# Kernel tuning notes

Measured on AMD Instinct MI355X. Metric: run time of the kernel, lower is better.

## Reference

```python
import jax, jax.numpy as jnp
import numpy as np

N = 4096
E_EDGES = 262144
F_IN = 128      # num_features
H = 4           # nhead (GAT heads and MHA heads)
C = 64          # d_model (per-head GAT out dim)
EMB = H * C     # 256, MHA embed_dim
DFF = 128       # dim_feedforward
HD = EMB // H   # MHA head dim = 64


def setup_inputs() -> dict:
    key = jax.random.key(0)
    ks = jax.random.split(key, 16)
    inp = {}
    inp["tgt"] = jax.random.normal(ks[0], (N, F_IN), jnp.float32)
    inp["memory"] = jax.random.normal(ks[1], (N, EMB), jnp.float32)
    inp["original_signal"] = jax.random.normal(ks[2], (N, EMB), jnp.float32)
    inp["edge_index"] = jax.random.randint(ks[3], (2, E_EDGES), 0, N, jnp.int32)
    # GATConv params (PyG: lin has no bias; separate bias of size H*C; att vectors [1,H,C])
    s = 1.0 / np.sqrt(F_IN)
    inp["W_gat"] = jax.random.normal(ks[4], (F_IN, H * C), jnp.float32) * s
    inp["att_src"] = jax.random.normal(ks[5], (H, C), jnp.float32) * (1.0 / np.sqrt(C))
    inp["att_dst"] = jax.random.normal(ks[6], (H, C), jnp.float32) * (1.0 / np.sqrt(C))
    inp["b_gat"] = jnp.zeros((H * C,), jnp.float32)
    # nn.MultiheadAttention params
    se = 1.0 / np.sqrt(EMB)
    inp["in_proj_w"] = jax.random.normal(ks[7], (3 * EMB, EMB), jnp.float32) * se
    inp["in_proj_b"] = jnp.zeros((3 * EMB,), jnp.float32)
    inp["out_proj_w"] = jax.random.normal(ks[8], (EMB, EMB), jnp.float32) * se
    inp["out_proj_b"] = jnp.zeros((EMB,), jnp.float32)
    # linear1
    inp["lin1_w"] = jax.random.normal(ks[9], (DFF, EMB), jnp.float32) * se
    inp["lin1_b"] = jnp.zeros((DFF,), jnp.float32)
    return inp


def _gat_conv(x, edge_index, W, att_src, att_dst, bias):
    n = x.shape[0]
    xh = (x @ W).reshape(n, H, C)                       # [N,H,C]
    a_s = jnp.sum(xh * att_src, axis=-1)                # [N,H]
    a_d = jnp.sum(xh * att_dst, axis=-1)                # [N,H]
    # add self loops (PyG default add_self_loops=True)
    loop = jnp.arange(n, dtype=edge_index.dtype)
    src = jnp.concatenate([edge_index[0], loop])
    dst = jnp.concatenate([edge_index[1], loop])
    alpha = jax.nn.leaky_relu(a_s[src] + a_d[dst], negative_slope=0.2)  # [E+N,H]
    # edge softmax grouped by destination node
    m = jax.ops.segment_max(alpha, dst, num_segments=n)
    alpha = jnp.exp(alpha - m[dst])
    denom = jax.ops.segment_sum(alpha, dst, num_segments=n)
    alpha = alpha / (denom[dst] + 1e-16)
    # message passing: weighted scatter-add of source features
    out = jax.ops.segment_sum(xh[src] * alpha[:, :, None], dst, num_segments=n)  # [N,H,C]
    return out.reshape(n, H * C) + bias


def _mha(q_in, k_in, v_in, in_proj_w, in_proj_b, out_proj_w, out_proj_b):
    # batch=1, seq=N; dropout inactive (eval)
    q = q_in @ in_proj_w[:EMB].T + in_proj_b[:EMB]
    k = k_in @ in_proj_w[EMB:2 * EMB].T + in_proj_b[EMB:2 * EMB]
    v = v_in @ in_proj_w[2 * EMB:].T + in_proj_b[2 * EMB:]
    q = q.reshape(-1, H, HD)
    k = k.reshape(-1, H, HD)
    v = v.reshape(-1, H, HD)
    scale = 1.0 / np.sqrt(HD)
    scores = jnp.einsum('nhd,mhd->hnm', q * scale, k)   # [H,N,N]
    attn = jax.nn.softmax(scores, axis=-1)
    o = jnp.einsum('hnm,mhd->nhd', attn, v).reshape(-1, EMB)
    return o @ out_proj_w.T + out_proj_b


def reference(tgt, memory, original_signal, edge_index,
              W_gat, att_src, att_dst, b_gat,
              in_proj_w, in_proj_b, out_proj_w, out_proj_b,
              lin1_w, lin1_b):
    t = _gat_conv(tgt, edge_index, W_gat, att_src, att_dst, b_gat)
    t = jax.nn.leaky_relu(t, negative_slope=0.01)       # F.leaky_relu default slope
    fused = _mha(t, memory, original_signal, in_proj_w, in_proj_b, out_proj_w, out_proj_b)
    return jax.nn.relu(fused @ lin1_w.T + lin1_b)       # [N, DFF]
```

## Files before the change

kernel.cpp:

```cpp
#include <hip/hip_runtime.h>

#define NN   4096
#define EE   262144
#define ET   (EE + NN)
#define HH   4
#define EMB  256
#define DFF  128
#define FIN  128
#define KSPLIT 8
#define KCHUNK (NN / KSPLIT)

typedef float  f32x16  __attribute__((ext_vector_type(16)));
typedef __bf16 bf16x8  __attribute__((ext_vector_type(8)));
typedef unsigned short u16;
typedef unsigned short u16x4 __attribute__((ext_vector_type(4)));

__device__ __forceinline__ u16 f2bf(float f) {
  unsigned u = __float_as_uint(f);
  u += 0x7fffu + ((u >> 16) & 1u);
  return (u16)(u >> 16);
}

__global__ __launch_bounds__(256) void gemm_f32(
    const float* __restrict__ A, const float* __restrict__ B,
    float* __restrict__ Cf, int M, int Nn, int K)
{
  __shared__ float As[64][17];
  __shared__ float Bs[16][65];
  const int tid = threadIdx.x;
  const int tr = tid >> 4, tc = tid & 15;
  const int m0 = blockIdx.y * 64, n0 = blockIdx.x * 64;
  float acc[4][4] = {};
  for (int k0 = 0; k0 < K; k0 += 16) {
    {
      const int r = tid >> 2, kq = (tid & 3) << 2;
      const float4 av = *(const float4*)(A + (size_t)(m0 + r) * K + k0 + kq);
      As[r][kq] = av.x; As[r][kq + 1] = av.y; As[r][kq + 2] = av.z; As[r][kq + 3] = av.w;
    }
    {
      const int kk = tid >> 4, jq = (tid & 15) << 2;
      const float4 bv = *(const float4*)(B + (size_t)(k0 + kk) * Nn + n0 + jq);
      Bs[kk][jq] = bv.x; Bs[kk][jq + 1] = bv.y; Bs[kk][jq + 2] = bv.z; Bs[kk][jq + 3] = bv.w;
    }
    __syncthreads();
#pragma unroll
    for (int kk = 0; kk < 16; ++kk) {
      float a[4], b[4];
#pragma unroll
      for (int i = 0; i < 4; ++i) a[i] = As[tr * 4 + i][kk];
#pragma unroll
      for (int j = 0; j < 4; ++j) b[j] = Bs[kk][tc * 4 + j];
#pragma unroll
      for (int i = 0; i < 4; ++i)
#pragma unroll
        for (int j = 0; j < 4; ++j) acc[i][j] += a[i] * b[j];
    }
    __syncthreads();
  }
#pragma unroll
  for (int i = 0; i < 4; ++i)
#pragma unroll
    for (int j = 0; j < 4; ++j)
      Cf[(size_t)(m0 + tr * 4 + i) * Nn + n0 + tc * 4 + j] = acc[i][j];
}

__global__ __launch_bounds__(256) void bgemm(
    const float* __restrict__ A, const float* __restrict__ B, const float* __restrict__ bias,
    float* __restrict__ Cf, int M, int Nn, int K, int act)
{
  __shared__ u16 As[64][40], Bs[64][40];
  const int tid = threadIdx.x;
  const int m0 = blockIdx.y * 64, n0 = blockIdx.x * 64;
  const int w = tid >> 6, l = tid & 63, lq = l & 31, hi = l >> 5;
  const int wm = w >> 1, wn = w & 1;
  f32x16 acc = {0};
  for (int k0 = 0; k0 < K; k0 += 32) {
    __syncthreads();
#pragma unroll
    for (int it = 0; it < 2; ++it) {
      const int idx = tid + it * 256;
      const int row = idx >> 3, slot = idx & 7;
      const float4 av = *(const float4*)(A + (size_t)(m0 + row) * K + k0 + slot * 4);
      u16x4 ap = {f2bf(av.x), f2bf(av.y), f2bf(av.z), f2bf(av.w)};
      *(u16x4*)(&As[row][slot * 4]) = ap;
      const float4 bv = *(const float4*)(B + (size_t)(n0 + row) * K + k0 + slot * 4);
      u16x4 bp = {f2bf(bv.x), f2bf(bv.y), f2bf(bv.z), f2bf(bv.w)};
      *(u16x4*)(&Bs[row][slot * 4]) = bp;
    }
    __syncthreads();
#pragma unroll
    for (int c = 0; c < 2; ++c) {
      const bf16x8 af = *(const bf16x8*)(&As[wm * 32 + lq][c * 16 + hi * 8]);
      const bf16x8 bf = *(const bf16x8*)(&Bs[wn * 32 + lq][c * 16 + hi * 8]);
      acc = __builtin_amdgcn_mfma_f32_32x32x16_bf16(af, bf, acc, 0, 0, 0);
    }
  }
  const int col = n0 + wn * 32 + lq;
  const float bcol = bias ? bias[col] : 0.f;
#pragma unroll
  for (int r = 0; r < 16; ++r) {
    const int row = m0 + wm * 32 + (r & 3) + 8 * (r >> 2) + 4 * hi;
    float v = acc[r] + bcol;
    if (act == 2) v = fmaxf(v, 0.f);
    Cf[(size_t)row * Nn + col] = v;
  }
}

__global__ __launch_bounds__(256) void qkv_mfma(
    const float* __restrict__ tbuf, const float* __restrict__ mem, const float* __restrict__ orig,
    const float* __restrict__ ipw, const float* __restrict__ ipb,
    u16* __restrict__ qb, u16* __restrict__ kbuf, u16* __restrict__ vT)
{
  __shared__ u16 As[64][40], Bs[64][40];
  const int z = blockIdx.z;
  const float* A = (z == 0) ? tbuf : (z == 1 ? mem : orig);
  const float* B = ipw + (size_t)z * EMB * EMB;
  const float* bias = ipb + z * EMB;
  const float oscale = (z == 0) ? 0.125f : 1.f;
  const int tid = threadIdx.x;
  const int m0 = blockIdx.y * 64, n0 = blockIdx.x * 64;
  const int w = tid >> 6, l = tid & 63, lq = l & 31, hi = l >> 5;
  const int wm = w >> 1, wn = w & 1;
  f32x16 acc = {0};
  for (int k0 = 0; k0 < EMB; k0 += 32) {
    __syncthreads();
#pragma unroll
    for (int it = 0; it < 2; ++it) {
      const int idx = tid + it * 256;
      const int row = idx >> 3, slot = idx & 7;
      const float4 av = *(const float4*)(A + (size_t)(m0 + row) * EMB + k0 + slot * 4);
      u16x4 ap = {f2bf(av.x), f2bf(av.y), f2bf(av.z), f2bf(av.w)};
      *(u16x4*)(&As[row][slot * 4]) = ap;
      const float4 bv = *(const float4*)(B + (size_t)(n0 + row) * EMB + k0 + slot * 4);
      u16x4 bp = {f2bf(bv.x), f2bf(bv.y), f2bf(bv.z), f2bf(bv.w)};
      *(u16x4*)(&Bs[row][slot * 4]) = bp;
    }
    __syncthreads();
#pragma unroll
    for (int c = 0; c < 2; ++c) {
      const bf16x8 af = *(const bf16x8*)(&As[wm * 32 + lq][c * 16 + hi * 8]);
      const bf16x8 bf = *(const bf16x8*)(&Bs[wn * 32 + lq][c * 16 + hi * 8]);
      acc = __builtin_amdgcn_mfma_f32_32x32x16_bf16(af, bf, acc, 0, 0, 0);
    }
  }
  const int col = n0 + wn * 32 + lq;
  const float bcol = bias[col];
  const int hh = col >> 6, dd = col & 63;
#pragma unroll
  for (int r = 0; r < 16; ++r) {
    const int row = m0 + wm * 32 + (r & 3) + 8 * (r >> 2) + 4 * hi;
    const u16 bw = f2bf((acc[r] + bcol) * oscale);
    if (z == 2) vT[((size_t)hh * 64 + dd) * NN + row] = bw;
    else if (z == 1) kbuf[((size_t)hh * NN + row) * 64 + dd] = bw;
    else qb[((size_t)hh * NN + row) * 64 + dd] = bw;
  }
}

__global__ __launch_bounds__(256) void att_sums(const float* __restrict__ xh,
                                                const float* __restrict__ att_src,
                                                const float* __restrict__ att_dst,
                                                float* __restrict__ a_s, float* __restrict__ a_d)
{
  const int n = blockIdx.x, t = threadIdx.x;
  const int h = t >> 6, c = t & 63;
  const float v = xh[(size_t)n * EMB + t];
  float s1 = v * att_src[t];
  float s2 = v * att_dst[t];
#pragma unroll
  for (int off = 32; off >= 1; off >>= 1) {
    s1 += __shfl_down(s1, off);
    s2 += __shfl_down(s2, off);
  }
  if (c == 0) { a_s[n * HH + h] = s1; a_d[n * HH + h] = s2; }
}

__global__ void edge_count(const int* __restrict__ ei, int* __restrict__ counts) {
  const int e = blockIdx.x * blockDim.x + threadIdx.x;
  if (e >= ET) return;
  const int dst = (e < EE) ? ei[EE + e] : (e - EE);
  atomicAdd(&counts[dst], 1);
}

__global__ __launch_bounds__(64) void scan4096(const int* __restrict__ counts, int* __restrict__ offs) {
  const int t = threadIdx.x;
  const int base = t * 64;
  int s = 0;
  for (int i = 0; i < 64; ++i) s += counts[base + i];
  int incl = s;
#pragma unroll
  for (int off = 1; off < 64; off <<= 1) {
    const int v = __shfl_up(incl, off);
    if (t >= off) incl += v;
  }
  int run = incl - s;
  for (int i = 0; i < 64; ++i) { offs[base + i] = run; run += counts[base + i]; }
}

__global__ void edge_scatter(const int* __restrict__ ei, const int* __restrict__ offs,
                             int* __restrict__ cursor, int* __restrict__ ssrc) {
  const int e = blockIdx.x * blockDim.x + threadIdx.x;
  if (e >= ET) return;
  int src, dst;
  if (e < EE) { src = ei[e]; dst = ei[EE + e]; } else { src = dst = e - EE; }
  const int pos = offs[dst] + atomicAdd(&cursor[dst], 1);
  ssrc[pos] = src;
}

__global__ __launch_bounds__(256) void gat_gather(
    const float* __restrict__ xh, const float* __restrict__ a_s, const float* __restrict__ a_d,
    const int* __restrict__ offs, const int* __restrict__ counts, const int* __restrict__ ssrc,
    const float* __restrict__ b_gat, float* __restrict__ t_out)
{
  const int dst = blockIdx.x, tid = threadIdx.x;
  const int h = tid >> 6, c = tid & 63;
  const float ad = a_d[dst * HH + h];
  const int beg = offs[dst], deg = counts[dst];
  float accv = 0.f, den = 0.f;
  for (int i = 0; i < deg; ++i) {
    const int src = ssrc[beg + i];
    float a = a_s[src * HH + h] + ad;
    a = a > 0.f ? a : 0.2f * a;
    const float p = __expf(a);
    den += p;
    accv += p * xh[(size_t)src * EMB + h * 64 + c];
  }
  float v = accv / (den + 1e-16f) + b_gat[tid];
  v = v > 0.f ? v : 0.01f * v;
  t_out[(size_t)dst * EMB + tid] = v;
}

__global__ __launch_bounds__(256) void flash32(
    const u16* __restrict__ qb, const u16* __restrict__ kb,
    const u16* __restrict__ vT, float* __restrict__ po,
    float* __restrict__ pm, float* __restrict__ pl)
{
  __shared__ float sld[4][32 * 33];
  const int h = blockIdx.y;
  const int qgroup = blockIdx.x / KSPLIT, ks = blockIdx.x % KSPLIT;
  const int w = threadIdx.x >> 6, l = threadIdx.x & 63;
  const int lq = l & 31, hi = l >> 5;
  const int qtile = qgroup * 4 + w;
  const int q0 = qtile * 32;
  const u16* qh = qb + (size_t)h * NN * 64;
  const u16* kh = kb + (size_t)h * NN * 64;
  const u16* vh = vT + (size_t)h * 64 * NN;

  bf16x8 qf[4];
#pragma unroll
  for (int c = 0; c < 4; ++c)
    qf[c] = *(const bf16x8*)(qh + (size_t)(q0 + lq) * 64 + c * 16 + hi * 8);

  f32x16 o0 = {0}, o1 = {0};
  float m_r = -1e30f, l_r = 0.f;

  const int kend = ks * KCHUNK + KCHUNK;
  for (int k0 = ks * KCHUNK; k0 < kend; k0 += 32) {
    f32x16 s = {0};
#pragma unroll
    for (int c = 0; c < 4; ++c) {
      const bf16x8 kf = *(const bf16x8*)(kh + (size_t)(k0 + lq) * 64 + c * 16 + hi * 8);
      s = __builtin_amdgcn_mfma_f32_32x32x16_bf16(kf, qf[c], s, 0, 0, 0);
    }
    float mx = s[0];
#pragma unroll
    for (int i = 1; i < 16; ++i) mx = fmaxf(mx, s[i]);
    const float colmax = fmaxf(mx, __shfl_xor(mx, 32));
    if (!__all(colmax <= m_r + 8.f)) {
      const float m_new = fmaxf(m_r, colmax);
      const float corr = __expf(m_r - m_new);
#pragma unroll
      for (int i = 0; i < 16; ++i) { o0[i] *= corr; o1[i] *= corr; }
      l_r *= corr;
      m_r = m_new;
    }
    float p[16];
    float ssum = 0.f;
#pragma unroll
    for (int i = 0; i < 16; ++i) { p[i] = __expf(s[i] - m_r); ssum += p[i]; }
    l_r += ssum + __shfl_xor(ssum, 32);

    unsigned wd[8];
#pragma unroll
    for (int i = 0; i < 8; ++i)
      wd[i] = (unsigned)f2bf(p[2 * i]) | ((unsigned)f2bf(p[2 * i + 1]) << 16);
    const unsigned t0 = __shfl_xor(hi ? wd[0] : wd[2], 32);
    const unsigned t1 = __shfl_xor(hi ? wd[1] : wd[3], 32);
    const unsigned t2 = __shfl_xor(hi ? wd[4] : wd[6], 32);
    const unsigned t3 = __shfl_xor(hi ? wd[5] : wd[7], 32);
    union { unsigned u[4]; bf16x8 b; } pf0, pf1;
    pf0.u[0] = hi ? t0 : wd[0];
    pf0.u[1] = hi ? t1 : wd[1];
    pf0.u[2] = hi ? wd[2] : t0;
    pf0.u[3] = hi ? wd[3] : t1;
    pf1.u[0] = hi ? t2 : wd[4];
    pf1.u[1] = hi ? t3 : wd[5];
    pf1.u[2] = hi ? wd[6] : t2;
    pf1.u[3] = hi ? wd[7] : t3;
    {
      const u16* vrow = vh + (size_t)lq * NN + k0 + hi * 8;
      const bf16x8 vf0 = *(const bf16x8*)(vrow);
      const bf16x8 vf1 = *(const bf16x8*)(vrow + 16);
      o0 = __builtin_amdgcn_mfma_f32_32x32x16_bf16(vf0, pf0.b, o0, 0, 0, 0);
      o0 = __builtin_amdgcn_mfma_f32_32x32x16_bf16(vf1, pf1.b, o0, 0, 0, 0);
    }
    {
      const u16* vrow = vh + (size_t)(32 + lq) * NN + k0 + hi * 8;
      const bf16x8 vf0 = *(const bf16x8*)(vrow);
      const bf16x8 vf1 = *(const bf16x8*)(vrow + 16);
      o1 = __builtin_amdgcn_mfma_f32_32x32x16_bf16(vf0, pf0.b, o1, 0, 0, 0);
      o1 = __builtin_amdgcn_mfma_f32_32x32x16_bf16(vf1, pf1.b, o1, 0, 0, 0);
    }
  }

  float* wld = sld[w];
  const size_t rowbase = (size_t)h * NN + q0;
  const int qq2 = (l >> 5), dd = l & 31;
#pragma unroll
  for (int r = 0; r < 16; ++r)
    wld[((r & 3) + 8 * (r >> 2) + 4 * hi) * 33 + lq] = o0[r];
#pragma unroll
  for (int qi = 0; qi < 16; ++qi) {
    const int qr = qi * 2 + qq2;
    po[(rowbase + qr) * (KSPLIT * 64) + ks * 64 + dd] = wld[dd * 33 + qr];
  }
#pragma unroll
  for (int r = 0; r < 16; ++r)
    wld[((r & 3) + 8 * (r >> 2) + 4 * hi) * 33 + lq] = o1[r];
#pragma unroll
  for (int qi = 0; qi < 16; ++qi) {
    const int qr = qi * 2 + qq2;
    po[(rowbase + qr) * (KSPLIT * 64) + ks * 64 + 32 + dd] = wld[dd * 33 + qr];
  }
  if (hi == 0) {
    const int pidx = (h * KSPLIT + ks) * NN + q0 + lq;
    pm[pidx] = m_r; pl[pidx] = l_r;
  }
}

__global__ __launch_bounds__(256) void combine2(
    const float* __restrict__ po, const float* __restrict__ pm,
    const float* __restrict__ pl, float* __restrict__ o)
{
  const int q = blockIdx.x;
  const int t = threadIdx.x;
  const int h = t >> 6, d = t & 63;
  float mloc[KSPLIT];
  float M = -1e30f;
#pragma unroll
  for (int i = 0; i < KSPLIT; ++i) {
    mloc[i] = pm[(h * KSPLIT + i) * NN + q];
    M = fmaxf(M, mloc[i]);
  }
  const size_t base = ((size_t)h * NN + q) * (KSPLIT * 64);
  float L = 0.f, acc = 0.f;
#pragma unroll
  for (int i = 0; i < KSPLIT; ++i) {
    const float wgt = __expf(mloc[i] - M);
    L += wgt * pl[(h * KSPLIT + i) * NN + q];
    acc += wgt * po[base + i * 64 + d];
  }
  o[(size_t)q * EMB + h * 64 + d] = acc / L;
}

extern "C" void kernel_launch(void* const* d_in, const int* in_sizes, int n_in,
                              void* d_out, int out_size, void* d_ws, size_t ws_size,
                              hipStream_t stream)
{
  const float* tgt   = (const float*)d_in[0];
  const float* mem   = (const float*)d_in[1];
  const float* orig  = (const float*)d_in[2];
  const int*   eidx  = (const int*)d_in[3];
  const float* Wg    = (const float*)d_in[4];
  const float* att_s = (const float*)d_in[5];
  const float* att_d = (const float*)d_in[6];
  const float* bg    = (const float*)d_in[7];
  const float* ipw   = (const float*)d_in[8];
  const float* ipb   = (const float*)d_in[9];
  const float* opw   = (const float*)d_in[10];
  const float* opb   = (const float*)d_in[11];
  const float* l1w   = (const float*)d_in[12];
  const float* l1b   = (const float*)d_in[13];
  float* out = (float*)d_out;

  char* ws = (char*)d_ws;
  size_t off = 0;
  auto alloc = [&](size_t bytes) -> void* {
    void* p = ws + off;
    off += (bytes + 255) & ~((size_t)255);
    return p;
  };
  float* xh    = (float*)alloc((size_t)NN * EMB * 4);
  float* tbuf  = (float*)alloc((size_t)NN * EMB * 4);
  float* a_s   = (float*)alloc((size_t)NN * HH * 4);
  float* a_d   = (float*)alloc((size_t)NN * HH * 4);
  int* counts  = (int*)alloc((size_t)NN * 4);
  int* offs    = (int*)alloc((size_t)NN * 4);
  int* cursor  = (int*)alloc((size_t)NN * 4);
  int* ssrc    = (int*)alloc((size_t)ET * 4);
  u16* qb      = (u16*)alloc((size_t)NN * EMB * 2);
  u16* kbuf    = (u16*)alloc((size_t)NN * EMB * 2);
  u16* vT      = (u16*)alloc((size_t)NN * EMB * 2);
  float* po    = (float*)alloc((size_t)HH * NN * KSPLIT * 64 * 4);
  float* pm    = (float*)alloc((size_t)HH * KSPLIT * NN * 4);
  float* pl    = (float*)alloc((size_t)HH * KSPLIT * NN * 4);
  float* obuf  = xh;
  float* fused = tbuf;

  (void)hipMemsetAsync(counts, 0, (size_t)NN * 4, stream);
  (void)hipMemsetAsync(cursor, 0, (size_t)NN * 4, stream);

  gemm_f32<<<dim3(EMB / 64, NN / 64), 256, 0, stream>>>(tgt, Wg, xh, NN, EMB, FIN);
  att_sums<<<NN, 256, 0, stream>>>(xh, att_s, att_d, a_s, a_d);
  edge_count<<<(ET + 255) / 256, 256, 0, stream>>>(eidx, counts);
  scan4096<<<1, 64, 0, stream>>>(counts, offs);
  edge_scatter<<<(ET + 255) / 256, 256, 0, stream>>>(eidx, offs, cursor, ssrc);
  gat_gather<<<NN, 256, 0, stream>>>(xh, a_s, a_d, offs, counts, ssrc, bg, tbuf);

  qkv_mfma<<<dim3(EMB / 64, NN / 64, 3), 256, 0, stream>>>(
      tbuf, mem, orig, ipw, ipb, qb, kbuf, vT);

  flash32<<<dim3(32 * KSPLIT, HH), 256, 0, stream>>>(qb, kbuf, vT, po, pm, pl);
  combine2<<<NN, 256, 0, stream>>>(po, pm, pl, obuf);

  bgemm<<<dim3(EMB / 64, NN / 64), 256, 0, stream>>>(
      obuf, opw, opb, fused, NN, EMB, EMB, 0);
  bgemm<<<dim3(DFF / 64, NN / 64), 256, 0, stream>>>(
      fused, l1w, l1b, out, NN, DFF, EMB, 2);
}
```

Before: 235.1 us.

## Use split-bf16 MFMA for GAT projection and exp2-based flash softmax

Replaces the scalar fp32 GAT projection GEMM with an MFMA kernel that splits each fp32 value into high and low bf16 parts and does three MFMAs, keeping near-fp32 accuracy while using matrix cores. In the flash attention kernel, log2(e) is folded into the Q scale so softmax uses exp2f. The kernel also uses tree reductions for the row max and sum, hardware bf16 pair packing, and loads V before the P shuffle so the MFMAs can be interleaved. Risks are extra LDS traffic and transposed scalar LDS stores in the new GEMM, plus small numeric differences.

```diff
diff --git a/kernel.cpp b/kernel.cpp
--- a/kernel.cpp
+++ b/kernel.cpp
@@ -1,4 +1,5 @@
 #include <hip/hip_runtime.h>
+#include <hip/hip_bf16.h>
 
 #define NN   4096
 #define EE   262144
@@ -15,53 +16,77 @@
 typedef unsigned short u16;
 typedef unsigned short u16x4 __attribute__((ext_vector_type(4)));
 
+#define LOG2E 1.4426950408889634f
+
 __device__ __forceinline__ u16 f2bf(float f) {
   unsigned u = __float_as_uint(f);
   u += 0x7fffu + ((u >> 16) & 1u);
   return (u16)(u >> 16);
 }
-
-__global__ __launch_bounds__(256) void gemm_f32(
+__device__ __forceinline__ unsigned split1(float x) {
+  const u16 h = f2bf(x);
+  const float hf = __uint_as_float(((unsigned)h) << 16);
+  const u16 l = f2bf(x - hf);
+  return (unsigned)h | ((unsigned)l << 16);
+}
+__device__ __forceinline__ unsigned pack_bf2(float a, float b) {
+  union { __hip_bfloat162 b2; unsigned u; } cv;
+  cv.b2 = __float22bfloat162_rn(make_float2(a, b));
+  return cv.u;
+}
+
+__global__ __launch_bounds__(256) void mgemm_nt(
     const float* __restrict__ A, const float* __restrict__ B,
     float* __restrict__ Cf, int M, int Nn, int K)
 {
-  __shared__ float As[64][17];
-  __shared__ float Bs[16][65];
+  __shared__ u16 Ah[64][40], Al[64][40], Bh[64][40], Bl[64][40];
   const int tid = threadIdx.x;
-  const int tr = tid >> 4, tc = tid & 15;
   const int m0 = blockIdx.y * 64, n0 = blockIdx.x * 64;
-  float acc[4][4] = {};
-  for (int k0 = 0; k0 < K; k0 += 16) {
-    {
-      const int r = tid >> 2, kq = (tid & 3) << 2;
-      const float4 av = *(const float4*)(A + (size_t)(m0 + r) * K + k0 + kq);
-      As[r][kq] = av.x; As[r][kq + 1] = av.y; As[r][kq + 2] = av.z; As[r][kq + 3] = av.w;
-    }
-    {
-      const int kk = tid >> 4, jq = (tid & 15) << 2;
-      const float4 bv = *(const float4*)(B + (size_t)(k0 + kk) * Nn + n0 + jq);
-      Bs[kk][jq] = bv.x; Bs[kk][jq + 1] = bv.y; Bs[kk][jq + 2] = bv.z; Bs[kk][jq + 3] = bv.w;
-    }
-    __syncthreads();
-#pragma unroll
-    for (int kk = 0; kk < 16; ++kk) {
-      float a[4], b[4];
-#pragma unroll
-      for (int i = 0; i < 4; ++i) a[i] = As[tr * 4 + i][kk];
-#pragma unroll
-      for (int j = 0; j < 4; ++j) b[j] = Bs[kk][tc * 4 + j];
-#pragma unroll
-      for (int i = 0; i < 4; ++i)
-#pragma unroll
-        for (int j = 0; j < 4; ++j) acc[i][j] += a[i] * b[j];
-    }
-    __syncthreads();
-  }
-#pragma unroll
-  for (int i = 0; i < 4; ++i)
-#pragma unroll
-    for (int j = 0; j < 4; ++j)
-      Cf[(size_t)(m0 + tr * 4 + i) * Nn + n0 + tc * 4 + j] = acc[i][j];
+  const int w = tid >> 6, l = tid & 63, lq = l & 31, hi = l >> 5;
+  const int wm = w >> 1, wn = w & 1;
+  f32x16 acc = {0};
+  for (int k0 = 0; k0 < K; k0 += 32) {
+    __syncthreads();
+#pragma unroll
+    for (int it = 0; it < 2; ++it) {
+      const int idx = tid + it * 256;
+      {
+        const int row = idx >> 3, slot = idx & 7;
+        const float4 av = *(const float4*)(A + (size_t)(m0 + row) * K + k0 + slot * 4);
+        const unsigned s0 = split1(av.x), s1 = split1(av.y), s2 = split1(av.z), s3 = split1(av.w);
+        u16x4 hp = {(u16)s0, (u16)s1, (u16)s2, (u16)s3};
+        u16x4 lp = {(u16)(s0 >> 16), (u16)(s1 >> 16), (u16)(s2 >> 16), (u16)(s3 >> 16)};
+        *(u16x4*)(&Ah[row][slot * 4]) = hp;
+        *(u16x4*)(&Al[row][slot * 4]) = lp;
+      }
+      {
+        const int kr = idx >> 4, nq = idx & 15;
+        const float4 bv = *(const float4*)(B + (size_t)(k0 + kr) * Nn + n0 + nq * 4);
+        const unsigned s0 = split1(bv.x), s1 = split1(bv.y), s2 = split1(bv.z), s3 = split1(bv.w);
+        Bh[nq * 4 + 0][kr] = (u16)s0; Bl[nq * 4 + 0][kr] = (u16)(s0 >> 16);
+        Bh[nq * 4 + 1][kr] = (u16)s1; Bl[nq * 4 + 1][kr] = (u16)(s1 >> 16);
+        Bh[nq * 4 + 2][kr] = (u16)s2; Bl[nq * 4 + 2][kr] = (u16)(s2 >> 16);
+        Bh[nq * 4 + 3][kr] = (u16)s3; Bl[nq * 4 + 3][kr] = (u16)(s3 >> 16);
+      }
+    }
+    __syncthreads();
+#pragma unroll
+    for (int c = 0; c < 2; ++c) {
+      const bf16x8 ah = *(const bf16x8*)(&Ah[wm * 32 + lq][c * 16 + hi * 8]);
+      const bf16x8 al = *(const bf16x8*)(&Al[wm * 32 + lq][c * 16 + hi * 8]);
+      const bf16x8 bh = *(const bf16x8*)(&Bh[wn * 32 + lq][c * 16 + hi * 8]);
+      const bf16x8 bl = *(const bf16x8*)(&Bl[wn * 32 + lq][c * 16 + hi * 8]);
+      acc = __builtin_amdgcn_mfma_f32_32x32x16_bf16(ah, bh, acc, 0, 0, 0);
+      acc = __builtin_amdgcn_mfma_f32_32x32x16_bf16(ah, bl, acc, 0, 0, 0);
+      acc = __builtin_amdgcn_mfma_f32_32x32x16_bf16(al, bh, acc, 0, 0, 0);
+    }
+  }
+  const int col = n0 + wn * 32 + lq;
+#pragma unroll
+  for (int r = 0; r < 16; ++r) {
+    const int row = m0 + wm * 32 + (r & 3) + 8 * (r >> 2) + 4 * hi;
+    Cf[(size_t)row * Nn + col] = acc[r];
+  }
 }
 
 __global__ __launch_bounds__(256) void bgemm(
@@ -116,7 +141,7 @@
   const float* A = (z == 0) ? tbuf : (z == 1 ? mem : orig);
   const float* B = ipw + (size_t)z * EMB * EMB;
   const float* bias = ipb + z * EMB;
-  const float oscale = (z == 0) ? 0.125f : 1.f;
+  const float oscale = (z == 0) ? (0.125f * LOG2E) : 1.f;
   const int tid = threadIdx.x;
   const int m0 = blockIdx.y * 64, n0 = blockIdx.x * 64;
   const int w = tid >> 6, l = tid & 63, lq = l & 31, hi = l >> 5;
@@ -261,28 +286,44 @@
       const bf16x8 kf = *(const bf16x8*)(kh + (size_t)(k0 + lq) * 64 + c * 16 + hi * 8);
       s = __builtin_amdgcn_mfma_f32_32x32x16_bf16(kf, qf[c], s, 0, 0, 0);
     }
-    float mx = s[0];
-#pragma unroll
-    for (int i = 1; i < 16; ++i) mx = fmaxf(mx, s[i]);
+    float tm[8];
+#pragma unroll
+    for (int i = 0; i < 8; ++i) tm[i] = fmaxf(s[2 * i], s[2 * i + 1]);
+#pragma unroll
+    for (int i = 0; i < 4; ++i) tm[i] = fmaxf(tm[i], tm[i + 4]);
+    tm[0] = fmaxf(tm[0], tm[2]); tm[1] = fmaxf(tm[1], tm[3]);
+    const float mx = fmaxf(tm[0], tm[1]);
     const float colmax = fmaxf(mx, __shfl_xor(mx, 32));
-    if (!__all(colmax <= m_r + 8.f)) {
+    if (!__all(colmax <= m_r + 11.54f)) {
       const float m_new = fmaxf(m_r, colmax);
-      const float corr = __expf(m_r - m_new);
+      const float corr = exp2f(m_r - m_new);
 #pragma unroll
       for (int i = 0; i < 16; ++i) { o0[i] *= corr; o1[i] *= corr; }
       l_r *= corr;
       m_r = m_new;
     }
     float p[16];
-    float ssum = 0.f;
-#pragma unroll
-    for (int i = 0; i < 16; ++i) { p[i] = __expf(s[i] - m_r); ssum += p[i]; }
+#pragma unroll
+    for (int i = 0; i < 16; ++i) p[i] = exp2f(s[i] - m_r);
+    float ts[8];
+#pragma unroll
+    for (int i = 0; i < 8; ++i) ts[i] = p[2 * i] + p[2 * i + 1];
+#pragma unroll
+    for (int i = 0; i < 4; ++i) ts[i] += ts[i + 4];
+    const float ssum = (ts[0] + ts[2]) + (ts[1] + ts[3]);
     l_r += ssum + __shfl_xor(ssum, 32);
 
+    const u16* vr0 = vh + (size_t)lq * NN + k0 + hi * 8;
+    const u16* vr1 = vh + (size_t)(32 + lq) * NN + k0 + hi * 8;
+    const bf16x8 vf00 = *(const bf16x8*)(vr0);
+    const bf16x8 vf01 = *(const bf16x8*)(vr0 + 16);
+    const bf16x8 vf10 = *(const bf16x8*)(vr1);
+    const bf16x8 vf11 = *(const bf16x8*)(vr1 + 16);
+
     unsigned wd[8];
 #pragma unroll
     for (int i = 0; i < 8; ++i)
-      wd[i] = (unsigned)f2bf(p[2 * i]) | ((unsigned)f2bf(p[2 * i + 1]) << 16);
+      wd[i] = pack_bf2(p[2 * i], p[2 * i + 1]);
     const unsigned t0 = __shfl_xor(hi ? wd[0] : wd[2], 32);
     const unsigned t1 = __shfl_xor(hi ? wd[1] : wd[3], 32);
     const unsigned t2 = __shfl_xor(hi ? wd[4] : wd[6], 32);
@@ -296,20 +337,10 @@
     pf1.u[1] = hi ? t3 : wd[5];
     pf1.u[2] = hi ? wd[6] : t2;
     pf1.u[3] = hi ? wd[7] : t3;
-    {
-      const u16* vrow = vh + (size_t)lq * NN + k0 + hi * 8;
-      const bf16x8 vf0 = *(const bf16x8*)(vrow);
-      const bf16x8 vf1 = *(const bf16x8*)(vrow + 16);
-      o0 = __builtin_amdgcn_mfma_f32_32x32x16_bf16(vf0, pf0.b, o0, 0, 0, 0);
-      o0 = __builtin_amdgcn_mfma_f32_32x32x16_bf16(vf1, pf1.b, o0, 0, 0, 0);
-    }
-    {
-      const u16* vrow = vh + (size_t)(32 + lq) * NN + k0 + hi * 8;
-      const bf16x8 vf0 = *(const bf16x8*)(vrow);
-      const bf16x8 vf1 = *(const bf16x8*)(vrow + 16);
-      o1 = __builtin_amdgcn_mfma_f32_32x32x16_bf16(vf0, pf0.b, o1, 0, 0, 0);
-      o1 = __builtin_amdgcn_mfma_f32_32x32x16_bf16(vf1, pf1.b, o1, 0, 0, 0);
-    }
+    o0 = __builtin_amdgcn_mfma_f32_32x32x16_bf16(vf00, pf0.b, o0, 0, 0, 0);
+    o1 = __builtin_amdgcn_mfma_f32_32x32x16_bf16(vf10, pf0.b, o1, 0, 0, 0);
+    o0 = __builtin_amdgcn_mfma_f32_32x32x16_bf16(vf01, pf1.b, o0, 0, 0, 0);
+    o1 = __builtin_amdgcn_mfma_f32_32x32x16_bf16(vf11, pf1.b, o1, 0, 0, 0);
   }
 
   float* wld = sld[w];
@@ -355,7 +386,7 @@
   float L = 0.f, acc = 0.f;
 #pragma unroll
   for (int i = 0; i < KSPLIT; ++i) {
-    const float wgt = __expf(mloc[i] - M);
+    const float wgt = exp2f(mloc[i] - M);
     L += wgt * pl[(h * KSPLIT + i) * NN + q];
     acc += wgt * po[base + i * 64 + d];
   }
@@ -409,7 +440,7 @@
   (void)hipMemsetAsync(counts, 0, (size_t)NN * 4, stream);
   (void)hipMemsetAsync(cursor, 0, (size_t)NN * 4, stream);
 
-  gemm_f32<<<dim3(EMB / 64, NN / 64), 256, 0, stream>>>(tgt, Wg, xh, NN, EMB, FIN);
+  mgemm_nt<<<dim3(EMB / 64, NN / 64), 256, 0, stream>>>(tgt, Wg, xh, NN, EMB, FIN);
   att_sums<<<NN, 256, 0, stream>>>(xh, att_s, att_d, a_s, a_d);
   edge_count<<<(ET + 255) / 256, 256, 0, stream>>>(eidx, counts);
   scan4096<<<1, 64, 0, stream>>>(counts, offs);
```

Measured after the change: 241.7 us. 1.03x slower.
